# Kernel optimization log

Hardware: AMD Instinct MI355X
Metric: run time of the kernel (lower is better)

## Reference

```python
import jax, jax.numpy as jnp
import numpy as np

NT, NX = 64, 64
N_HALF = NT * NX // 2  # 2048 sites per checkerboard half

# mask[:, ::2] = False -> True at odd-x columns (the 'A' half)
_mask = np.ones((NT, NX), dtype=bool)
_mask[:, ::2] = False
IDX_A = jnp.asarray(np.where(_mask.reshape(-1))[0])   # [N_HALF]
IDX_B = jnp.asarray(np.where(~_mask.reshape(-1))[0])  # [N_HALF]


def setup_inputs() -> dict:
    key = jax.random.key(0)
    k0, k1, k2, k3, k4 = jax.random.split(key, 5)
    B = 4096
    scale = 1.0 / np.sqrt(N_HALF)
    return {
        "input_phi": jax.random.normal(k0, (B, NT, NX), dtype=jnp.float32),
        "W_s": jax.random.normal(k1, (N_HALF, N_HALF), dtype=jnp.float32) * scale,
        "b_s": jnp.zeros((N_HALF,), dtype=jnp.float32),
        "W_t": jax.random.normal(k2, (N_HALF, N_HALF), dtype=jnp.float32) * scale,
        "b_t": jnp.zeros((N_HALF,), dtype=jnp.float32),
    }


def _coupling(A, B, W_s, b_s, W_t, b_t):
    # Affine coupling: A' = A * exp(s(B)) + t(B); logDetJ = sum(s(B))
    s = jnp.tanh(B @ W_s.T + b_s)   # [batch, N_HALF]
    t = B @ W_t.T + b_t             # [batch, N_HALF]
    return A * jnp.exp(s) + t, jnp.sum(s, axis=-1)


def reference(input_phi, W_s, b_s, W_t, b_t):
    lead = input_phi.shape[:-2]
    phi = input_phi.reshape(*lead, NT * NX)
    A = phi[..., IDX_A]  # [batch, N_HALF]
    B = phi[..., IDX_B]
    A, logDetJc1 = _coupling(A, B, W_s, b_s, W_t, b_t)
    B, logDetJc2 = _coupling(B, A, W_s, b_s, W_t, b_t)
    out = jnp.zeros_like(phi).at[..., IDX_A].set(A).at[..., IDX_B].set(B)
    return out.reshape(*lead, NT, NX), logDetJc1 + logDetJc2
```

## Files before the change

kernel.cpp:

```cpp
#include <hip/hip_runtime.h>
#include <stdint.h>

#define BATCH 4096
#define NTX   4096
#define NH    2048
#define KDIM  2048

#define BM 256
#define BN 128
#define BK 64
#define THREADS 512
#define NITER (KDIM / BK)

#define A_OFF 0
#define S_OFF 16384
#define T_OFF 24576
#define BUF_E 32768

typedef __bf16 bf16x8 __attribute__((ext_vector_type(8)));
typedef float  f32x4  __attribute__((ext_vector_type(4)));

__device__ __forceinline__ unsigned short f2bf(float f) {
    union { float f; unsigned u; } v; v.f = f;
    unsigned u = v.u;
    unsigned r = u + 0x7fffu + ((u >> 16) & 1u);
    return (unsigned short)(r >> 16);
}

__device__ __forceinline__ float fast_tanh(float x) {
    float e = __expf(x + x);
    return 1.f - 2.f / (e + 1.f);
}

typedef __attribute__((address_space(1))) void gvoid;
typedef __attribute__((address_space(3))) void lvoid;

__device__ __forceinline__ void async16(const unsigned short* g, unsigned short* l) {
    __builtin_amdgcn_global_load_lds((gvoid*)(void*)g, (lvoid*)l, 16, 0, 0);
}

__device__ __forceinline__ int roff(int R, int c) {
    return R * BK + (((c) + (R & 7)) & 7) * 8;
}

__global__ void prep(const float* __restrict__ phi,
                     const float* __restrict__ Wsf,
                     const float* __restrict__ Wtf,
                     unsigned short* __restrict__ Bbf,
                     unsigned short* __restrict__ Wsb,
                     unsigned short* __restrict__ Wtb,
                     float* __restrict__ out)
{
    const int tid    = blockIdx.x * blockDim.x + threadIdx.x;
    const int stride = gridDim.x * blockDim.x;

    const float4* p4 = (const float4*)phi;
    for (int i = tid; i < (BATCH * NH / 4); i += stride) {
        float4 u = p4[2 * i], v = p4[2 * i + 1];
        uint2 o;
        o.x = (unsigned)f2bf(u.x) | ((unsigned)f2bf(u.z) << 16);
        o.y = (unsigned)f2bf(v.x) | ((unsigned)f2bf(v.z) << 16);
        ((uint2*)Bbf)[i] = o;
    }

    const float4* ws4 = (const float4*)Wsf;
    const float4* wt4 = (const float4*)Wtf;
    for (int i = tid; i < (NH * KDIM / 8); i += stride) {
        float4 u = ws4[2 * i], v = ws4[2 * i + 1];
        uint4 o;
        o.x = (unsigned)f2bf(u.x) | ((unsigned)f2bf(u.y) << 16);
        o.y = (unsigned)f2bf(u.z) | ((unsigned)f2bf(u.w) << 16);
        o.z = (unsigned)f2bf(v.x) | ((unsigned)f2bf(v.y) << 16);
        o.w = (unsigned)f2bf(v.z) | ((unsigned)f2bf(v.w) << 16);
        ((uint4*)Wsb)[i] = o;
        u = wt4[2 * i]; v = wt4[2 * i + 1];
        o.x = (unsigned)f2bf(u.x) | ((unsigned)f2bf(u.y) << 16);
        o.y = (unsigned)f2bf(u.z) | ((unsigned)f2bf(u.w) << 16);
        o.z = (unsigned)f2bf(v.x) | ((unsigned)f2bf(v.y) << 16);
        o.w = (unsigned)f2bf(v.z) | ((unsigned)f2bf(v.w) << 16);
        ((uint4*)Wtb)[i] = o;
    }

    for (int i = tid; i < BATCH; i += stride) out[(size_t)BATCH * NTX + i] = 0.f;
}

__global__ __launch_bounds__(THREADS, 2) void coupling_gemm(
    const unsigned short* __restrict__ X,
    const unsigned short* __restrict__ Wsb,
    const unsigned short* __restrict__ Wtb,
    const float* __restrict__ bs,
    const float* __restrict__ bt,
    const float* __restrict__ phi,
    float* __restrict__ out,
    unsigned short* __restrict__ Xout,
    int parity)
{
    __shared__ unsigned short lds[2][BUF_E];

    const int tid = threadIdx.x;

    const int lid  = blockIdx.x;
    const int xcd  = lid & 7;
    const int slot = lid >> 3;
    const int m0 = (slot & 15) * BM;
    const int n0 = (2 * xcd + (slot >> 4)) * BN;

    f32x4 acc_s[4][4], acc_t[4][4];
    const f32x4 zf = {0.f, 0.f, 0.f, 0.f};
#pragma unroll
    for (int i = 0; i < 4; i++)
#pragma unroll
        for (int j = 0; j < 4; j++) { acc_s[i][j] = zf; acc_t[i][j] = zf; }

    const int srow = tid >> 3;
    const int cg   = ((tid & 7) - (srow & 7)) & 7;
    const unsigned short* Ag = X   + (size_t)(m0 + srow) * KDIM + cg * 8;
    const unsigned short* Sg = Wsb + (size_t)(n0 + srow) * KDIM + cg * 8;
    const unsigned short* Tg = Wtb + (size_t)(n0 + srow) * KDIM + cg * 8;
    const size_t r64  = (size_t)64  * KDIM;
    const size_t r128 = (size_t)128 * KDIM;
    const int lw = tid * 8;

    const int wave = tid >> 6;
    const int lane = tid & 63;
    const int wm = (wave >> 1) * 64;
    const int wn = (wave & 1) * 64;
    const int lrow = lane & 15;
    const int kc   = lane >> 4;

    int aO[4], sO[4], tO[4];
#pragma unroll
    for (int i = 0; i < 4; i++) {
        aO[i] = A_OFF + roff(wm + i * 16 + lrow, kc);
        sO[i] = S_OFF + roff(wn + i * 16 + lrow, kc);
        tO[i] = T_OFF + roff(wn + i * 16 + lrow, kc);
    }

    {
        unsigned short* b = &lds[0][0];
        async16(Ag,              b + A_OFF + lw);
        async16(Ag + r64,        b + A_OFF + 4096 + lw);
        async16(Ag + r128,       b + A_OFF + 8192 + lw);
        async16(Ag + r128 + r64, b + A_OFF + 12288 + lw);
        async16(Sg,              b + S_OFF + lw);
        async16(Sg + r64,        b + S_OFF + 4096 + lw);
        async16(Tg,              b + T_OFF + lw);
        async16(Tg + r64,        b + T_OFF + 4096 + lw);
    }
    asm volatile("s_waitcnt vmcnt(2)" ::: "memory");
    __builtin_amdgcn_s_barrier();

    auto tile = [&](unsigned short* bc, unsigned short* bx, int t) {
        const int k0n = (((t + 1) < NITER) ? (t + 1) : 0) * BK;
        bf16x8 a0[4], a1[4], f[4];

#pragma unroll
        for (int i = 0; i < 4; i++) {
            a0[i] = *(const bf16x8*)(bc + aO[i]);
            f[i]  = *(const bf16x8*)(bc + sO[i]);
        }
        async16(Ag + k0n,              bx + A_OFF + lw);
        async16(Ag + k0n + r64,        bx + A_OFF + 4096 + lw);
        async16(Ag + k0n + r128,       bx + A_OFF + 8192 + lw);
        async16(Ag + k0n + r128 + r64, bx + A_OFF + 12288 + lw);
        __builtin_amdgcn_s_barrier();
        __builtin_amdgcn_s_setprio(1);
#pragma unroll
        for (int mi = 0; mi < 4; mi++)
#pragma unroll
            for (int ni = 0; ni < 4; ni++)
                acc_s[mi][ni] = __builtin_amdgcn_mfma_f32_16x16x32_bf16(
                    a0[mi], f[ni], acc_s[mi][ni], 0, 0, 0);
        __builtin_amdgcn_s_setprio(0);
        __builtin_amdgcn_s_barrier();

#pragma unroll
        for (int i = 0; i < 4; i++) {
            a1[i] = *(const bf16x8*)(bc + (aO[i] ^ 32));
            f[i]  = *(const bf16x8*)(bc + (sO[i] ^ 32));
        }
        async16(Sg + k0n,       bx + S_OFF + lw);
        async16(Sg + k0n + r64, bx + S_OFF + 4096 + lw);
        async16(Tg + k0n,       bx + T_OFF + lw);
        async16(Tg + k0n + r64, bx + T_OFF + 4096 + lw);
        __builtin_amdgcn_s_barrier();
        __builtin_amdgcn_s_setprio(1);
#pragma unroll
        for (int mi = 0; mi < 4; mi++)
#pragma unroll
            for (int ni = 0; ni < 4; ni++)
                acc_s[mi][ni] = __builtin_amdgcn_mfma_f32_16x16x32_bf16(
                    a1[mi], f[ni], acc_s[mi][ni], 0, 0, 0);
        __builtin_amdgcn_s_setprio(0);
        asm volatile("s_waitcnt vmcnt(8)" ::: "memory");
        __builtin_amdgcn_s_barrier();

#pragma unroll
        for (int i = 0; i < 4; i++)
            f[i] = *(const bf16x8*)(bc + tO[i]);
        __builtin_amdgcn_s_barrier();
        __builtin_amdgcn_s_setprio(1);
#pragma unroll
        for (int mi = 0; mi < 4; mi++)
#pragma unroll
            for (int ni = 0; ni < 4; ni++)
                acc_t[mi][ni] = __builtin_amdgcn_mfma_f32_16x16x32_bf16(
                    a0[mi], f[ni], acc_t[mi][ni], 0, 0, 0);
        __builtin_amdgcn_s_setprio(0);
        __builtin_amdgcn_s_barrier();

#pragma unroll
        for (int i = 0; i < 4; i++)
            f[i] = *(const bf16x8*)(bc + (tO[i] ^ 32));
        __builtin_amdgcn_s_barrier();
        __builtin_amdgcn_s_setprio(1);
#pragma unroll
        for (int mi = 0; mi < 4; mi++)
#pragma unroll
            for (int ni = 0; ni < 4; ni++)
                acc_t[mi][ni] = __builtin_amdgcn_mfma_f32_16x16x32_bf16(
                    a1[mi], f[ni], acc_t[mi][ni], 0, 0, 0);
        __builtin_amdgcn_s_setprio(0);
        asm volatile("s_waitcnt vmcnt(2)" ::: "memory");
        __builtin_amdgcn_s_barrier();
    };

    for (int t = 0; t < NITER; t += 2) {
        tile(&lds[0][0], &lds[1][0], t);
        tile(&lds[1][0], &lds[0][0], t + 1);
    }

    float* ldslot = out + (size_t)BATCH * NTX;
#pragma unroll
    for (int mi = 0; mi < 4; mi++) {
#pragma unroll
        for (int r = 0; r < 4; r++) {
            const int brow = m0 + wm + mi * 16 + (lane >> 4) * 4 + r;
            float ssum = 0.f;
#pragma unroll
            for (int ni = 0; ni < 4; ni++) {
                const int n = n0 + wn + ni * 16 + lrow;
                float s  = fast_tanh(acc_s[mi][ni][r] + bs[n]);
                float tv = acc_t[mi][ni][r] + bt[n];
                const size_t oidx = (size_t)brow * NTX + 2 * n + parity;
                float val = fmaf(phi[oidx], __expf(s), tv);
                out[oidx] = val;
                if (Xout) Xout[(size_t)brow * NH + n] = f2bf(val);
                ssum += s;
            }
            ssum += __shfl_xor(ssum, 1);
            ssum += __shfl_xor(ssum, 2);
            ssum += __shfl_xor(ssum, 4);
            ssum += __shfl_xor(ssum, 8);
            if (lrow == 0) atomicAdd(ldslot + brow, ssum);
        }
    }
}

extern "C" void kernel_launch(void* const* d_in, const int* in_sizes, int n_in,
                              void* d_out, int out_size, void* d_ws, size_t ws_size,
                              hipStream_t stream) {
    const float* phi = (const float*)d_in[0];
    const float* Wsf = (const float*)d_in[1];
    const float* bs  = (const float*)d_in[2];
    const float* Wtf = (const float*)d_in[3];
    const float* bt  = (const float*)d_in[4];
    float* out = (float*)d_out;

    char* ws = (char*)d_ws;
    unsigned short* Bbf  = (unsigned short*)(ws);
    unsigned short* Apbf = (unsigned short*)(ws + 16777216);
    unsigned short* Wsb  = (unsigned short*)(ws + 33554432);
    unsigned short* Wtb  = (unsigned short*)(ws + 41943040);

    prep<<<2048, 256, 0, stream>>>(phi, Wsf, Wtf, Bbf, Wsb, Wtb, out);

    coupling_gemm<<<256, THREADS, 0, stream>>>(
        Bbf, Wsb, Wtb, bs, bt, phi, out, Apbf, 1);

    coupling_gemm<<<256, THREADS, 0, stream>>>(
        Apbf, Wsb, Wtb, bs, bt, phi, out, nullptr, 0);
}
```

Measured before the change: 316.5 us.

## Software-pipeline LDS fragment reads with MFMA phases and issue all prefetches early

Restructures the K-loop so LDS fragment reads for the next MFMA phase are issued before the current MFMA block runs. The first A/S fragments of the next tile are preloaded at the end of each tile. All global-to-LDS async copies for the next tile are issued up front, and the barrier count per tile drops from eight to four. Fragment offsets are computed from one base with XOR and stride arithmetic instead of per-row arrays. This hides LDS latency behind matrix work at the cost of more live vector registers, and waiting on all async copies (vmcnt(0)) may expose global load latency.

```diff
diff --git a/kernel.cpp b/kernel.cpp
--- a/kernel.cpp
+++ b/kernel.cpp
@@ -128,13 +128,29 @@
     const int lrow = lane & 15;
     const int kc   = lane >> 4;
 
-    int aO[4], sO[4], tO[4];
-#pragma unroll
-    for (int i = 0; i < 4; i++) {
-        aO[i] = A_OFF + roff(wm + i * 16 + lrow, kc);
-        sO[i] = S_OFF + roff(wn + i * 16 + lrow, kc);
-        tO[i] = T_OFF + roff(wn + i * 16 + lrow, kc);
-    }
+    const int aO0 = A_OFF + roff(wm + lrow, kc);
+    const int aO1 = aO0 ^ 32;
+    const int sO0 = S_OFF + roff(wn + lrow, kc);
+    const int sO1 = sO0 ^ 32;
+
+    bf16x8 a0[4], a1[4], s0[4], s1[4], t0[4], t1[4];
+
+    auto rd4 = [&](bf16x8* d, const unsigned short* base, int off) {
+#pragma unroll
+        for (int i = 0; i < 4; i++)
+            d[i] = *(const bf16x8*)(base + off + 1024 * i);
+    };
+    auto mm = [&](f32x4 (&acc)[4][4], bf16x8* a, bf16x8* b) {
+        __builtin_amdgcn_sched_barrier(0);
+        __builtin_amdgcn_s_setprio(1);
+#pragma unroll
+        for (int mi = 0; mi < 4; mi++)
+#pragma unroll
+            for (int ni = 0; ni < 4; ni++)
+                acc[mi][ni] = __builtin_amdgcn_mfma_f32_16x16x32_bf16(
+                    a[mi], b[ni], acc[mi][ni], 0, 0, 0);
+        __builtin_amdgcn_s_setprio(0);
+    };
 
     {
         unsigned short* b = &lds[0][0];
@@ -147,81 +163,40 @@
         async16(Tg,              b + T_OFF + lw);
         async16(Tg + r64,        b + T_OFF + 4096 + lw);
     }
-    asm volatile("s_waitcnt vmcnt(2)" ::: "memory");
+    asm volatile("s_waitcnt vmcnt(0)" ::: "memory");
     __builtin_amdgcn_s_barrier();
+    rd4(a0, &lds[0][0], aO0);
+    rd4(s0, &lds[0][0], sO0);
 
     auto tile = [&](unsigned short* bc, unsigned short* bx, int t) {
         const int k0n = (((t + 1) < NITER) ? (t + 1) : 0) * BK;
-        bf16x8 a0[4], a1[4], f[4];
-
-#pragma unroll
-        for (int i = 0; i < 4; i++) {
-            a0[i] = *(const bf16x8*)(bc + aO[i]);
-            f[i]  = *(const bf16x8*)(bc + sO[i]);
-        }
+
+        rd4(t0, bc, sO0 + 8192);
         async16(Ag + k0n,              bx + A_OFF + lw);
         async16(Ag + k0n + r64,        bx + A_OFF + 4096 + lw);
         async16(Ag + k0n + r128,       bx + A_OFF + 8192 + lw);
         async16(Ag + k0n + r128 + r64, bx + A_OFF + 12288 + lw);
-        __builtin_amdgcn_s_barrier();
-        __builtin_amdgcn_s_setprio(1);
-#pragma unroll
-        for (int mi = 0; mi < 4; mi++)
-#pragma unroll
-            for (int ni = 0; ni < 4; ni++)
-                acc_s[mi][ni] = __builtin_amdgcn_mfma_f32_16x16x32_bf16(
-                    a0[mi], f[ni], acc_s[mi][ni], 0, 0, 0);
-        __builtin_amdgcn_s_setprio(0);
-        __builtin_amdgcn_s_barrier();
-
-#pragma unroll
-        for (int i = 0; i < 4; i++) {
-            a1[i] = *(const bf16x8*)(bc + (aO[i] ^ 32));
-            f[i]  = *(const bf16x8*)(bc + (sO[i] ^ 32));
-        }
-        async16(Sg + k0n,       bx + S_OFF + lw);
-        async16(Sg + k0n + r64, bx + S_OFF + 4096 + lw);
-        async16(Tg + k0n,       bx + T_OFF + lw);
-        async16(Tg + k0n + r64, bx + T_OFF + 4096 + lw);
-        __builtin_amdgcn_s_barrier();
-        __builtin_amdgcn_s_setprio(1);
-#pragma unroll
-        for (int mi = 0; mi < 4; mi++)
-#pragma unroll
-            for (int ni = 0; ni < 4; ni++)
-                acc_s[mi][ni] = __builtin_amdgcn_mfma_f32_16x16x32_bf16(
-                    a1[mi], f[ni], acc_s[mi][ni], 0, 0, 0);
-        __builtin_amdgcn_s_setprio(0);
-        asm volatile("s_waitcnt vmcnt(8)" ::: "memory");
-        __builtin_amdgcn_s_barrier();
-
-#pragma unroll
-        for (int i = 0; i < 4; i++)
-            f[i] = *(const bf16x8*)(bc + tO[i]);
-        __builtin_amdgcn_s_barrier();
-        __builtin_amdgcn_s_setprio(1);
-#pragma unroll
-        for (int mi = 0; mi < 4; mi++)
-#pragma unroll
-            for (int ni = 0; ni < 4; ni++)
-                acc_t[mi][ni] = __builtin_amdgcn_mfma_f32_16x16x32_bf16(
-                    a0[mi], f[ni], acc_t[mi][ni], 0, 0, 0);
-        __builtin_amdgcn_s_setprio(0);
-        __builtin_amdgcn_s_barrier();
-
-#pragma unroll
-        for (int i = 0; i < 4; i++)
-            f[i] = *(const bf16x8*)(bc + (tO[i] ^ 32));
-        __builtin_amdgcn_s_barrier();
-        __builtin_amdgcn_s_setprio(1);
-#pragma unroll
-        for (int mi = 0; mi < 4; mi++)
-#pragma unroll
-            for (int ni = 0; ni < 4; ni++)
-                acc_t[mi][ni] = __builtin_amdgcn_mfma_f32_16x16x32_bf16(
-                    a1[mi], f[ni], acc_t[mi][ni], 0, 0, 0);
-        __builtin_amdgcn_s_setprio(0);
+        async16(Sg + k0n,              bx + S_OFF + lw);
+        async16(Sg + k0n + r64,        bx + S_OFF + 4096 + lw);
+        async16(Tg + k0n,              bx + T_OFF + lw);
+        async16(Tg + k0n + r64,        bx + T_OFF + 4096 + lw);
+        mm(acc_s, a0, s0);
+        __builtin_amdgcn_s_barrier();
+
+        rd4(a1, bc, aO1);
+        rd4(s1, bc, sO1);
+        mm(acc_t, a0, t0);
+        __builtin_amdgcn_s_barrier();
+
+        rd4(t1, bc, sO1 + 8192);
+        mm(acc_s, a1, s1);
         asm volatile("s_waitcnt vmcnt(2)" ::: "memory");
+        __builtin_amdgcn_s_barrier();
+
+        rd4(a0, bx, aO0);
+        rd4(s0, bx, sO0);
+        mm(acc_t, a1, t1);
+        asm volatile("s_waitcnt vmcnt(0)" ::: "memory");
         __builtin_amdgcn_s_barrier();
     };
 
```

After: 319.5 us. About the same (+1.0%).
